# Performance work log

Hardware: AMD Instinct MI355X
Metric: run time of the kernel (lower is better)

The kernel has to match this reference:

```python
import jax, jax.numpy as jnp
import numpy as np
import math

DIM = 512


def setup_inputs() -> dict:
    key = jax.random.key(0)
    ks = jax.random.split(key, 6)
    B, N, D = 4, 4096, DIM
    H = D // 2
    features = jax.random.normal(ks[0], (B, N, D), dtype=jnp.float32)
    W1 = jax.random.normal(ks[1], (D, H), dtype=jnp.float32) * 0.02
    b1 = jnp.zeros((H,), dtype=jnp.float32)
    ln_g = jnp.ones((H,), dtype=jnp.float32)
    ln_b = jnp.zeros((H,), dtype=jnp.float32)
    W2 = jax.random.normal(ks[2], (H, 1), dtype=jnp.float32) * 0.02
    b2 = jnp.zeros((1,), dtype=jnp.float32)
    target_entropy = jnp.ones((1,), dtype=jnp.float32) * math.log(D)
    temperature = jnp.ones((1,), dtype=jnp.float32)
    return {"features": features, "W1": W1, "b1": b1, "ln_g": ln_g,
            "ln_b": ln_b, "W2": W2, "b2": b2,
            "target_entropy": target_entropy, "temperature": temperature}


def _layernorm(x, g, b, eps=1e-5):
    mu = jnp.mean(x, axis=-1, keepdims=True)
    var = jnp.mean((x - mu) ** 2, axis=-1, keepdims=True)
    return (x - mu) * jax.lax.rsqrt(var + eps) * g + b


def reference(features, W1, b1, ln_g, ln_b, W2, b2, target_entropy, temperature):
    # ---- compute_entropy: pairwise RBF kernel over [B, N, D] ----
    sq = jnp.sum(features ** 2, axis=-1)                       # [B, N]
    gram = jnp.einsum('bnd,bmd->bnm', features, features)      # [B, N, N]
    d2 = jnp.maximum(sq[:, :, None] + sq[:, None, :] - 2.0 * gram, 0.0)
    tau = temperature[0]
    kernel = jnp.exp(-d2 / (2.0 * tau ** 2))                   # [B, N, N]
    probs = kernel / jnp.sum(kernel, axis=-1, keepdims=True)
    entropy = -jnp.sum(probs * jnp.log(probs + 1e-6), axis=-1)  # [B, N]

    # ---- entropy estimator MLP (computed in original forward, output unused) ----
    h = features @ W1 + b1
    h = _layernorm(h, ln_g, ln_b)
    h = jax.nn.gelu(h, approximate=False)
    estimated_entropy = h @ W2 + b2                            # [B, N, 1] (unused)
    del estimated_entropy

    # ---- sigmoid-gated control signal ----
    entropy_diff = entropy - target_entropy[0]
    control_signal = jax.nn.sigmoid(-entropy_diff / tau)       # [B, N]
    controlled_features = features * control_signal[..., None]
    return controlled_features, control_signal
```

## Files before the change

### kernel.cpp

```cpp
#include <hip/hip_runtime.h>
#include <stdint.h>

#define N_TOK 4096
#define DIM   512
#define BATCH 4
#define BN    (BATCH * N_TOK)
#define JSPLIT 8
#define IPW   64
#define IPB   256
#define NG    (N_TOK / JSPLIT / 16)

typedef __attribute__((ext_vector_type(4))) float f32x4;

__device__ __forceinline__ float sumsq8(uint lo, uint hi) {
    float s = 0.f, f;
    f = __builtin_amdgcn_cvt_f32_fp8((int)lo, 0); s = fmaf(f, f, s);
    f = __builtin_amdgcn_cvt_f32_fp8((int)lo, 1); s = fmaf(f, f, s);
    f = __builtin_amdgcn_cvt_f32_fp8((int)lo, 2); s = fmaf(f, f, s);
    f = __builtin_amdgcn_cvt_f32_fp8((int)lo, 3); s = fmaf(f, f, s);
    f = __builtin_amdgcn_cvt_f32_fp8((int)hi, 0); s = fmaf(f, f, s);
    f = __builtin_amdgcn_cvt_f32_fp8((int)hi, 1); s = fmaf(f, f, s);
    f = __builtin_amdgcn_cvt_f32_fp8((int)hi, 2); s = fmaf(f, f, s);
    f = __builtin_amdgcn_cvt_f32_fp8((int)hi, 3); s = fmaf(f, f, s);
    return s;
}

__global__ __launch_bounds__(256) void prep_kernel(
    const float* __restrict__ feat, uint8_t* __restrict__ fb,
    uint8_t* __restrict__ fbT, float* __restrict__ sq)
{
    __shared__ __align__(16) long lt[1024];
    const int t = threadIdx.x;
    const int row16 = t >> 4, seg = t & 15;
    const size_t grp = blockIdx.x;
    const size_t row = grp * 16 + row16;

    const float4* src = (const float4*)(feat + row * DIM + seg * 32);
    uint32_t wd[8];
    float s = 0.f;
#pragma unroll
    for (int i = 0; i < 4; ++i) {
        float4 a = src[2 * i], b = src[2 * i + 1];
        uint lo = (uint)__builtin_amdgcn_cvt_pk_fp8_f32(a.x, a.y, 0, false);
        lo      = (uint)__builtin_amdgcn_cvt_pk_fp8_f32(a.z, a.w, (int)lo, true);
        uint hi = (uint)__builtin_amdgcn_cvt_pk_fp8_f32(b.x, b.y, 0, false);
        hi      = (uint)__builtin_amdgcn_cvt_pk_fp8_f32(b.z, b.w, (int)hi, true);
        wd[2 * i] = lo; wd[2 * i + 1] = hi;
        s += sumsq8(lo, hi);
    }

    uint4* dst = (uint4*)(fb + row * DIM + seg * 32);
    uint4 o0; o0.x = wd[0]; o0.y = wd[1]; o0.z = wd[2]; o0.w = wd[3];
    uint4 o1; o1.x = wd[4]; o1.y = wd[5]; o1.z = wd[6]; o1.w = wd[7];
    dst[0] = o0; dst[1] = o1;

#pragma unroll
    for (int i = 0; i < 4; ++i) {
        int c = seg * 4 + i;
        long d = ((long)(unsigned)wd[2 * i + 1] << 32) | (unsigned)wd[2 * i];
        lt[c * 16 + ((row16 + c) & 15)] = d;
    }

#pragma unroll
    for (int m = 1; m < 16; m <<= 1) s += __shfl_xor(s, m);
    if (seg == 0) sq[row] = s;

    __syncthreads();
    long* ot = (long*)(fbT + grp * 8192);
#pragma unroll
    for (int i = 0; i < 4; ++i) {
        int p    = t + i * 256;
        int kp   = p >> 7;
        int q    = (p >> 5) & 3;
        int r    = (p >> 1) & 15;
        int half = p & 1;
        int c    = (((kp << 1) | half) << 2) | q;
        ot[p] = lt[c * 16 + ((r + c) & 15)];
    }
}

__global__ __launch_bounds__(256, 2) void entropy_kernel(
    const uint8_t* __restrict__ fb, const uint8_t* __restrict__ fbT,
    const float* __restrict__ sq, const float* __restrict__ temp,
    float* __restrict__ Sp, float* __restrict__ Tp)
{
    const int t    = threadIdx.x;
    const int w    = t >> 6;
    const int lane = t & 63;
    const int q    = lane >> 4;
    const int c16  = lane & 15;

    const int flat  = blockIdx.x;
    const int combo = flat & 31;
    const int batch = combo >> 3;
    const int jh    = combo & 7;
    const int iblk  = flat >> 5;
    const int iw    = iblk * IPB + w * IPW;
    const size_t rowbase = (size_t)batch * N_TOK;

    const float tau    = temp[0];
    const float inv2t2 = 0.5f / (tau * tau);
    const float cg     = 1.0f / (tau * tau);

    long afrag[4][16];
#pragma unroll
    for (int s = 0; s < 4; ++s) {
        const long* ap = (const long*)(fb + (rowbase + iw + s * 16 + c16) * DIM);
#pragma unroll
        for (int kc = 0; kc < 16; ++kc) afrag[s][kc] = ap[kc * 4 + q];
    }
    float pi[4][4];
#pragma unroll
    for (int s = 0; s < 4; ++s)
#pragma unroll
        for (int r = 0; r < 4; ++r)
            pi[s][r] = -sq[rowbase + iw + s * 16 + q * 4 + r] * inv2t2;

    float S[4][4], T[4][4];
#pragma unroll
    for (int s = 0; s < 4; ++s)
#pragma unroll
        for (int r = 0; r < 4; ++r) { S[s][r] = 0.f; T[s][r] = 0.f; }

    const longlong2* bp = (const longlong2*)(fbT
                        + ((size_t)batch * (N_TOK / 16) + (size_t)jh * NG) * 8192) + lane;
    const float* sqj = sq + rowbase + jh * (N_TOK / JSPLIT) + c16;

    for (int g = 0; g < NG; ++g) {
        float pj = -sqj[g * 16] * inv2t2;
        const longlong2* bg = bp + (size_t)g * 512;
        f32x4 acc[4] = {{0,0,0,0},{0,0,0,0},{0,0,0,0},{0,0,0,0}};
#pragma unroll
        for (int kp = 0; kp < 8; ++kp) {
            longlong2 v = bg[kp * 64];
            acc[0] = __builtin_amdgcn_mfma_f32_16x16x32_fp8_fp8(afrag[0][2*kp],   v.x, acc[0], 0, 0, 0);
            acc[1] = __builtin_amdgcn_mfma_f32_16x16x32_fp8_fp8(afrag[1][2*kp],   v.x, acc[1], 0, 0, 0);
            acc[2] = __builtin_amdgcn_mfma_f32_16x16x32_fp8_fp8(afrag[2][2*kp],   v.x, acc[2], 0, 0, 0);
            acc[3] = __builtin_amdgcn_mfma_f32_16x16x32_fp8_fp8(afrag[3][2*kp],   v.x, acc[3], 0, 0, 0);
            acc[0] = __builtin_amdgcn_mfma_f32_16x16x32_fp8_fp8(afrag[0][2*kp+1], v.y, acc[0], 0, 0, 0);
            acc[1] = __builtin_amdgcn_mfma_f32_16x16x32_fp8_fp8(afrag[1][2*kp+1], v.y, acc[1], 0, 0, 0);
            acc[2] = __builtin_amdgcn_mfma_f32_16x16x32_fp8_fp8(afrag[2][2*kp+1], v.y, acc[2], 0, 0, 0);
            acc[3] = __builtin_amdgcn_mfma_f32_16x16x32_fp8_fp8(afrag[3][2*kp+1], v.y, acc[3], 0, 0, 0);
        }
        float m = -1e30f;
#pragma unroll
        for (int s = 0; s < 4; ++s)
#pragma unroll
            for (int r = 0; r < 4; ++r) {
                acc[s][r] = fmaf(acc[s][r], cg, pi[s][r] + pj);
                m = fmaxf(m, acc[s][r]);
            }
        if (m > -110.0f) {
#pragma unroll
            for (int s = 0; s < 4; ++s)
#pragma unroll
                for (int r = 0; r < 4; ++r) {
                    float ee = fminf(acc[s][r], 0.f);
                    float k  = __expf(ee);
                    S[s][r] += k;
                    T[s][r]  = fmaf(k, ee, T[s][r]);
                }
        }
    }

#pragma unroll
    for (int m = 1; m < 16; m <<= 1)
#pragma unroll
        for (int s = 0; s < 4; ++s)
#pragma unroll
            for (int r = 0; r < 4; ++r) {
                S[s][r] += __shfl_xor(S[s][r], m);
                T[s][r] += __shfl_xor(T[s][r], m);
            }

    if (c16 == 0) {
#pragma unroll
        for (int s = 0; s < 4; ++s)
#pragma unroll
            for (int r = 0; r < 4; ++r) {
                size_t idx = (size_t)jh * BN + rowbase + iw + s * 16 + q * 4 + r;
                Sp[idx] = S[s][r];
                Tp[idx] = T[s][r];
            }
    }
}

__global__ __launch_bounds__(256) void finalize_kernel(
    const float* __restrict__ feat, const float* __restrict__ Sp,
    const float* __restrict__ Tp, const float* __restrict__ tgt,
    const float* __restrict__ temp, float* __restrict__ out)
{
    int row  = (blockIdx.x << 2) + (threadIdx.x >> 6);
    int lane = threadIdx.x & 63;
    float S = 0.0f, T = 0.0f;
#pragma unroll
    for (int j = 0; j < JSPLIT; ++j) {
        S += Sp[(size_t)j * BN + row];
        T += Tp[(size_t)j * BN + row];
    }
    float tau = temp[0];
    float E  = __logf(S) - T / S;
    float cs = 1.0f / (1.0f + __expf((E - tgt[0]) / tau));

    const float4* F4 = (const float4*)(feat + (size_t)row * DIM);
    float4*       O4 = (float4*)(out + (size_t)row * DIM);
    float4 v0 = F4[lane], v1 = F4[lane + 64];
    v0.x *= cs; v0.y *= cs; v0.z *= cs; v0.w *= cs;
    v1.x *= cs; v1.y *= cs; v1.z *= cs; v1.w *= cs;
    O4[lane] = v0; O4[lane + 64] = v1;
    if (lane == 0) out[(size_t)BN * DIM + row] = cs;
}

extern "C" void kernel_launch(void* const* d_in, const int* in_sizes, int n_in,
                              void* d_out, int out_size, void* d_ws, size_t ws_size,
                              hipStream_t stream) {
    const float* feat = (const float*)d_in[0];
    const float* tgt  = (const float*)d_in[7];
    const float* temp = (const float*)d_in[8];
    float* out = (float*)d_out;

    char* ws = (char*)d_ws;
    uint8_t* fb  = (uint8_t*)ws;
    uint8_t* fbT = fb + (size_t)BN * DIM;
    float*   sq  = (float*)(fbT + (size_t)BN * DIM);
    float*   Sp  = sq + BN;
    float*   Tp  = Sp + (size_t)JSPLIT * BN;

    prep_kernel<<<dim3(BN / 16), dim3(256), 0, stream>>>(feat, fb, fbT, sq);
    entropy_kernel<<<dim3((N_TOK / IPB) * BATCH * JSPLIT), dim3(256), 0, stream>>>(fb, fbT, sq, temp, Sp, Tp);
    finalize_kernel<<<dim3(BN / 4), dim3(256), 0, stream>>>(feat, Sp, Tp, tgt, temp, out);
}
```

Before: 168.3 us.

## Exploit symmetry of RBF kernel matrix by computing only upper-triangular tile pairs

The pairwise kernel matrix is symmetric, so each block now handles one (ti, tj) tile pair with tj >= ti and skips the lower triangle. Off-diagonal tiles add their column sums into the j rows through atomics, alongside the row sums for the i rows. Partial-sum buffers are replaced by one atomically accumulated S/T array, zeroed with a memset and read directly in finalize. This roughly halves the MFMA and exp work at the cost of many global float atomics, per-tile cross-lane reductions and a nondeterministic summation order.

```diff
diff --git a/kernel.cpp b/kernel.cpp
--- a/kernel.cpp
+++ b/kernel.cpp
@@ -5,10 +5,11 @@
 #define DIM   512
 #define BATCH 4
 #define BN    (BATCH * N_TOK)
-#define JSPLIT 8
+#define NTILE 16
+#define NPAIR (NTILE * (NTILE + 1) / 2)
 #define IPW   64
 #define IPB   256
-#define NG    (N_TOK / JSPLIT / 16)
+#define NG    16
 
 typedef __attribute__((ext_vector_type(4))) float f32x4;
 
@@ -90,12 +91,13 @@
     const int q    = lane >> 4;
     const int c16  = lane & 15;
 
-    const int flat  = blockIdx.x;
-    const int combo = flat & 31;
-    const int batch = combo >> 3;
-    const int jh    = combo & 7;
-    const int iblk  = flat >> 5;
-    const int iw    = iblk * IPB + w * IPW;
+    int ti = 0, rem = blockIdx.x;
+    while (rem >= NTILE - ti) { rem -= NTILE - ti; ++ti; }
+    const int  tj   = ti + rem;
+    const bool diag = (ti == tj);
+
+    const int batch = blockIdx.y;
+    const int iw    = ti * IPB + w * IPW;
     const size_t rowbase = (size_t)batch * N_TOK;
 
     const float tau    = temp[0];
@@ -123,8 +125,8 @@
         for (int r = 0; r < 4; ++r) { S[s][r] = 0.f; T[s][r] = 0.f; }
 
     const longlong2* bp = (const longlong2*)(fbT
-                        + ((size_t)batch * (N_TOK / 16) + (size_t)jh * NG) * 8192) + lane;
-    const float* sqj = sq + rowbase + jh * (N_TOK / JSPLIT) + c16;
+                        + ((size_t)batch * (N_TOK / 16) + (size_t)tj * NG) * 8192) + lane;
+    const float* sqj = sq + rowbase + tj * IPB + c16;
 
     for (int g = 0; g < NG; ++g) {
         float pj = -sqj[g * 16] * inv2t2;
@@ -151,15 +153,25 @@
                 m = fmaxf(m, acc[s][r]);
             }
         if (m > -110.0f) {
+            float cs = 0.f, ct = 0.f;
 #pragma unroll
             for (int s = 0; s < 4; ++s)
 #pragma unroll
                 for (int r = 0; r < 4; ++r) {
                     float ee = fminf(acc[s][r], 0.f);
                     float k  = __expf(ee);
-                    S[s][r] += k;
-                    T[s][r]  = fmaf(k, ee, T[s][r]);
+                    S[s][r] += k;  T[s][r] = fmaf(k, ee, T[s][r]);
+                    cs      += k;  ct      = fmaf(k, ee, ct);
                 }
+            if (!diag) {
+                cs += __shfl_xor(cs, 16); cs += __shfl_xor(cs, 32);
+                ct += __shfl_xor(ct, 16); ct += __shfl_xor(ct, 32);
+                if (q == 0) {
+                    size_t jrow = rowbase + (size_t)tj * IPB + g * 16 + c16;
+                    atomicAdd(&Sp[jrow], cs);
+                    atomicAdd(&Tp[jrow], ct);
+                }
+            }
         }
     }
 
@@ -172,15 +184,14 @@
                 S[s][r] += __shfl_xor(S[s][r], m);
                 T[s][r] += __shfl_xor(T[s][r], m);
             }
-
     if (c16 == 0) {
 #pragma unroll
         for (int s = 0; s < 4; ++s)
 #pragma unroll
             for (int r = 0; r < 4; ++r) {
-                size_t idx = (size_t)jh * BN + rowbase + iw + s * 16 + q * 4 + r;
-                Sp[idx] = S[s][r];
-                Tp[idx] = T[s][r];
+                size_t idx = rowbase + iw + s * 16 + q * 4 + r;
+                atomicAdd(&Sp[idx], S[s][r]);
+                atomicAdd(&Tp[idx], T[s][r]);
             }
     }
 }
@@ -192,12 +203,7 @@
 {
     int row  = (blockIdx.x << 2) + (threadIdx.x >> 6);
     int lane = threadIdx.x & 63;
-    float S = 0.0f, T = 0.0f;
-#pragma unroll
-    for (int j = 0; j < JSPLIT; ++j) {
-        S += Sp[(size_t)j * BN + row];
-        T += Tp[(size_t)j * BN + row];
-    }
+    float S = Sp[row], T = Tp[row];
     float tau = temp[0];
     float E  = __logf(S) - T / S;
     float cs = 1.0f / (1.0f + __expf((E - tgt[0]) / tau));
@@ -224,9 +230,10 @@
     uint8_t* fbT = fb + (size_t)BN * DIM;
     float*   sq  = (float*)(fbT + (size_t)BN * DIM);
     float*   Sp  = sq + BN;
-    float*   Tp  = Sp + (size_t)JSPLIT * BN;
-
+    float*   Tp  = Sp + BN;
+
+    hipMemsetAsync(Sp, 0, 2 * (size_t)BN * sizeof(float), stream);
     prep_kernel<<<dim3(BN / 16), dim3(256), 0, stream>>>(feat, fb, fbT, sq);
-    entropy_kernel<<<dim3((N_TOK / IPB) * BATCH * JSPLIT), dim3(256), 0, stream>>>(fb, fbT, sq, temp, Sp, Tp);
+    entropy_kernel<<<dim3(NPAIR, BATCH), dim3(256), 0, stream>>>(fb, fbT, sq, temp, Sp, Tp);
     finalize_kernel<<<dim3(BN / 4), dim3(256), 0, stream>>>(feat, Sp, Tp, tgt, temp, out);
 }
```

Result: slower. 178.3 us (+6.0%).
